# Kernel tuning notes

Measured on AMD Instinct MI355X. Metric: run time of the kernel, lower is better.

Reference implementation:

```python
import jax, jax.numpy as jnp
import numpy as np

D = 1024; H = 16; DH = 64; L = 4; N0 = 512; N1 = 512; NF = 16; B = 4; FF = 2730
FUSION = -1; GLOBAL = -2

# static token-type masks (zorro=True path)
_tt = np.concatenate([np.zeros(N0, np.int64), np.ones(N1, np.int64), np.full(NF, FUSION, np.int64)])
_allowed = (_tt[:, None] == _tt[None, :]) | (_tt[:, None] == FUSION)
ATTN_MASK = jnp.asarray(~_allowed)  # True = masked, shape [N, N]
_rt = np.array([0, 1, FUSION, GLOBAL], np.int64)
_pool_allowed = (_rt[:, None] == _tt[None, :]) | (_rt[:, None] == GLOBAL)
POOL_MASK = jnp.asarray(~_pool_allowed)  # [4, N]


def setup_inputs() -> dict:
    key = jax.random.key(0)
    ks = jax.random.split(key, 14)
    s = 0.02
    return {
        'm0': jax.random.normal(ks[0], (B, N0, D), jnp.float32),
        'm1': jax.random.normal(ks[1], (B, N1, D), jnp.float32),
        'fusion_tokens': jax.random.normal(ks[2], (NF, D), jnp.float32),
        'return_tokens': jax.random.normal(ks[3], (4, D), jnp.float32),
        'ln_gamma': jnp.ones((L, D), jnp.float32),
        'wq': jax.random.normal(ks[4], (L, D, H * DH), jnp.float32) * s,
        'wkv': jax.random.normal(ks[5], (L, D, 2 * H * DH), jnp.float32) * s,
        'wo': jax.random.normal(ks[6], (L, H * DH, D), jnp.float32) * s,
        'ff_w1': jax.random.normal(ks[7], (L, D, 2 * FF), jnp.float32) * s,
        'ff_w2': jax.random.normal(ks[8], (L, FF, D), jnp.float32) * s,
        'pool_wq': jax.random.normal(ks[9], (D, H * DH), jnp.float32) * s,
        'pool_wkv': jax.random.normal(ks[10], (D, 2 * H * DH), jnp.float32) * s,
        'pool_wo': jax.random.normal(ks[11], (H * DH, D), jnp.float32) * s,
        'final_gamma': jnp.ones((D,), jnp.float32),
    }


def _ln(x, g):
    mu = jnp.mean(x, axis=-1, keepdims=True)
    var = jnp.mean(jnp.square(x - mu), axis=-1, keepdims=True)
    return (x - mu) * jax.lax.rsqrt(var + 1e-5) * g


def _heads(t):  # [b, n, h*d] -> [b, h, n, d]
    b, n, _ = t.shape
    return t.reshape(b, n, H, DH).transpose(0, 2, 1, 3)


def _attn(x, ctx, wq, wkv, wo, mask):
    q = _heads(x @ wq) * (DH ** -0.5)
    k, v = map(_heads, jnp.split(ctx @ wkv, 2, axis=-1))
    sim = jnp.einsum('bhid,bhjd->bhij', q, k)
    sim = jnp.where(mask, -jnp.finfo(sim.dtype).max, sim)
    attn = jax.nn.softmax(sim, axis=-1)
    out = jnp.einsum('bhij,bhjd->bhid', attn, v)
    b, h, n, d = out.shape
    return out.transpose(0, 2, 1, 3).reshape(b, n, h * d) @ wo


def _ff(x, w1, w2):
    val, gate = jnp.split(x @ w1, 2, axis=-1)
    return (jax.nn.gelu(gate, approximate=False) * val) @ w2


def reference(m0, m1, fusion_tokens, return_tokens, ln_gamma, wq, wkv, wo, ff_w1, ff_w2, pool_wq, pool_wkv, pool_wo, final_gamma):
    b = m0.shape[0]
    fus = jnp.broadcast_to(fusion_tokens[None], (b, NF, D))
    tokens = jnp.concatenate([m0, m1, fus], axis=1)  # [B, N, D]
    for l in range(L):
        h = _ln(tokens, ln_gamma[l])
        tokens = _attn(h, h, wq[l], wkv[l], wo[l], ATTN_MASK) + tokens
        h = _ln(tokens, ln_gamma[l])
        tokens = _ff(h, ff_w1[l], ff_w2[l]) + tokens
    tokens = _ln(tokens, final_gamma)
    q = jnp.broadcast_to(return_tokens[None], (b, 4, D))
    pooled = _attn(q, tokens, pool_wq, pool_wkv, pool_wo, POOL_MASK) + return_tokens[None]
    return pooled
```

## Files before the change

kernel.cpp:

```cpp
#include <hip/hip_runtime.h>
#include <stdint.h>


#define DEV __device__ __forceinline__

typedef unsigned short u16;
typedef __attribute__((ext_vector_type(8))) __bf16 bf16x8;
typedef __attribute__((ext_vector_type(4))) float floatx4;

DEV u16 f2bf(float f) {
  union { float f; unsigned u; } v; v.f = f;
  return (u16)((v.u + 0x7fffu + ((v.u >> 16) & 1u)) >> 16);
}
DEV float bf2f(u16 s) {
  union { unsigned u; float f; } v; v.u = ((unsigned)s) << 16;
  return v.f;
}

#define MFMA(a, b, c) __builtin_amdgcn_mfma_f32_16x16x32_bf16(a, b, c, 0, 0, 0)

DEV void gld16(const u16* g, u16* l) {
  __builtin_amdgcn_global_load_lds((__attribute__((address_space(1))) void*)g,
                                   (__attribute__((address_space(3))) void*)l,
                                   16, 0, 0);
}

DEV int vperm32(int j) {
  return (((j >> 2) & 3) << 3) | (j & 3) | (((j >> 4) & 1) << 2);
}

#define MREAL 4160
#define MPAD  4224
#define NPAD  1056
#define FFP   2816
#define FF2P  5632

__global__ __launch_bounds__(256) void transpose_cvt(
    const float* __restrict__ in, u16* __restrict__ out,
    int Kin, int N, int Kstride) {
  __shared__ float tile[32][33];
  const int k0 = blockIdx.x * 32, n0 = blockIdx.y * 32;
  const int tx = threadIdx.x, ty = threadIdx.y;
#pragma unroll
  for (int i = 0; i < 4; i++) {
    int k = k0 + ty + i * 8;
    tile[ty + i * 8][tx] = (k < Kin) ? in[(int64_t)k * N + n0 + tx] : 0.f;
  }
  __syncthreads();
#pragma unroll
  for (int i = 0; i < 4; i++) {
    int n = n0 + ty + i * 8;
    int k = k0 + tx;
    if (k < Kstride) out[(int64_t)n * Kstride + k] = f2bf(tile[tx][ty + i * 8]);
  }
}

__global__ __launch_bounds__(256) void transpose_w1(
    const float* __restrict__ in, u16* __restrict__ out) {
  __shared__ float tile[32][33];
  const int k0 = blockIdx.x * 32;
  const int r0 = blockIdx.y * 32;
  const int tx = threadIdx.x, ty = threadIdx.y;
  const int vb = (r0 >> 5) << 4;
  const int vi = vb + (tx & 15);
  const int c = (tx < 16) ? vi : 2730 + vi;
  const bool valid = vi < 2730;
#pragma unroll
  for (int i = 0; i < 4; i++) {
    int k = k0 + ty + i * 8;
    tile[ty + i * 8][tx] = valid ? in[(int64_t)k * 5460 + c] : 0.f;
  }
  __syncthreads();
#pragma unroll
  for (int i = 0; i < 4; i++) {
    int rl = ty + i * 8;
    out[(int64_t)(r0 + rl) * 1024 + k0 + tx] = f2bf(tile[tx][rl]);
  }
}

__global__ __launch_bounds__(256) void build_tokens_k(
    const float* __restrict__ m0p, const float* __restrict__ m1p,
    const float* __restrict__ fus, float* __restrict__ tokens) {
  const int n = blockIdx.x, b = blockIdx.y, t = threadIdx.x;
  const float* src = (n < 512) ? m0p + ((int64_t)b * 512 + n) * 1024
                   : (n < 1024) ? m1p + ((int64_t)b * 512 + (n - 512)) * 1024
                                : fus + (int64_t)(n - 1024) * 1024;
  float4 v = ((const float4*)src)[t];
  ((float4*)(tokens + ((int64_t)b * 1040 + n) * 1024))[t] = v;
}

__global__ __launch_bounds__(256) void ln_k(const float* __restrict__ x,
                                            const float* __restrict__ gamma,
                                            u16* __restrict__ out) {
  const int r = blockIdx.x, t = threadIdx.x;
  const float4 v = ((const float4*)(x + (int64_t)r * 1024))[t];
  float s = v.x + v.y + v.z + v.w;
  float q = v.x * v.x + v.y * v.y + v.z * v.z + v.w * v.w;
#pragma unroll
  for (int off = 32; off >= 1; off >>= 1) {
    s += __shfl_xor(s, off);
    q += __shfl_xor(q, off);
  }
  __shared__ float red[8];
  const int w = t >> 6, l = t & 63;
  if (l == 0) { red[w] = s; red[4 + w] = q; }
  __syncthreads();
  s = red[0] + red[1] + red[2] + red[3];
  q = red[4] + red[5] + red[6] + red[7];
  const float mu = s * (1.f / 1024.f);
  const float var = q * (1.f / 1024.f) - mu * mu;
  const float rs = rsqrtf(var + 1e-5f);
  const float4 g = ((const float4*)gamma)[t];
  u16* op = out + (int64_t)r * 1024 + t * 4;
  op[0] = f2bf((v.x - mu) * rs * g.x);
  op[1] = f2bf((v.y - mu) * rs * g.y);
  op[2] = f2bf((v.z - mu) * rs * g.z);
  op[3] = f2bf((v.w - mu) * rs * g.w);
}

enum { EPI_QKV = 0, EPI_KV = 1, EPI_TOKADD = 2, EPI_GG = 3 };

template <int EPI>
__global__ __launch_bounds__(256) void gemm_bt(
    const u16* __restrict__ A, const u16* __restrict__ Bt,
    int Kstr, int Mreal,
    float* __restrict__ tokens, u16* __restrict__ oq, u16* __restrict__ ok,
    u16* __restrict__ ovT, u16* __restrict__ oh2) {
  __shared__ __align__(16) u16 lA0[128 * 32];
  __shared__ __align__(16) u16 lA1[128 * 32];
  __shared__ __align__(16) u16 lB0[128 * 32];
  __shared__ __align__(16) u16 lB1[128 * 32];
  const int t = threadIdx.x;
  const int w = t >> 6, l = t & 63;
  const int lane16 = l & 15, quad = l >> 4;
  const int m0 = blockIdx.y * 128, n0 = blockIdx.x * 128;
  const int wm = (w >> 1) * 64, wn = (w & 1) * 64;

  const int Klen = Kstr / gridDim.z;
  const int koff = blockIdx.z * Klen;

  const floatx4 fz = {0.f, 0.f, 0.f, 0.f};
  floatx4 acc[4][4];
#pragma unroll
  for (int i = 0; i < 4; i++)
#pragma unroll
    for (int j = 0; j < 4; j++) acc[i][j] = fz;

  const int rowL = t >> 2;
  const int colL = (t & 3) * 8;
  const u16* gA = A + (int64_t)(m0 + rowL) * Kstr + koff + colL;
  const u16* gB = Bt + (int64_t)(n0 + rowL) * Kstr + koff + colL;
  u16* lA0p = lA0 + t * 8;
  u16* lA1p = lA1 + t * 8;
  u16* lB0p = lB0 + t * 8;
  u16* lB1p = lB1 + t * 8;
  const int fo = (wm + lane16) * 32 + quad * 8;
  const int fon = (wn + lane16) * 32 + quad * 8;
  const int64_t rsk = (int64_t)64 * Kstr;

  for (int kt = 0; kt < Klen; kt += 64) {
    gld16(gA + kt, lA0p);
    gld16(gA + kt + rsk, lA0p + 64 * 32);
    gld16(gA + kt + 32, lA1p);
    gld16(gA + kt + 32 + rsk, lA1p + 64 * 32);
    gld16(gB + kt, lB0p);
    gld16(gB + kt + rsk, lB0p + 64 * 32);
    gld16(gB + kt + 32, lB1p);
    gld16(gB + kt + 32 + rsk, lB1p + 64 * 32);
    __syncthreads();
    bf16x8 af[4], bf[4];
#pragma unroll
    for (int i = 0; i < 4; i++) af[i] = *(const bf16x8*)(lA0 + fo + i * 16 * 32);
#pragma unroll
    for (int j = 0; j < 4; j++) bf[j] = *(const bf16x8*)(lB0 + fon + j * 16 * 32);
#pragma unroll
    for (int i = 0; i < 4; i++)
#pragma unroll
      for (int j = 0; j < 4; j++) acc[i][j] = MFMA(af[i], bf[j], acc[i][j]);
#pragma unroll
    for (int i = 0; i < 4; i++) af[i] = *(const bf16x8*)(lA1 + fo + i * 16 * 32);
#pragma unroll
    for (int j = 0; j < 4; j++) bf[j] = *(const bf16x8*)(lB1 + fon + j * 16 * 32);
#pragma unroll
    for (int i = 0; i < 4; i++)
#pragma unroll
      for (int j = 0; j < 4; j++) acc[i][j] = MFMA(af[i], bf[j], acc[i][j]);
    __syncthreads();
  }

  if constexpr (EPI == EPI_TOKADD) {
    const bool atomic = gridDim.z > 1;
#pragma unroll
    for (int i = 0; i < 4; i++) {
      const int mb = m0 + wm + i * 16 + quad * 4;
#pragma unroll
      for (int reg = 0; reg < 4; reg++) {
        const int m = mb + reg;
        if (m < Mreal) {
          float* tp = tokens + (int64_t)m * 1024;
#pragma unroll
          for (int j = 0; j < 4; j++) {
            const int n = n0 + wn + j * 16 + lane16;
            if (atomic) atomicAdd(tp + n, acc[i][j][reg]);
            else tp[n] += acc[i][j][reg];
          }
        }
      }
    }
  } else if constexpr (EPI == EPI_QKV) {
#pragma unroll
    for (int i = 0; i < 4; i++) {
      const int mb = m0 + wm + i * 16 + quad * 4;
#pragma unroll
      for (int reg = 0; reg < 4; reg++) {
        const int m = mb + reg;
        if (m < Mreal) {
          const int b = m / 1040, rb = m % 1040;
          const int rbp = (rb & ~31) | vperm32(rb & 31);
#pragma unroll
          for (int j = 0; j < 4; j++) {
            const int n = n0 + wn + j * 16 + lane16;
            const float v = acc[i][j][reg];
            if (n < 1024) {
              const int hd = n >> 6, d = n & 63;
              oq[(((int64_t)b * 16 + hd) * NPAD + rb) * 64 + d] = f2bf(v * 0.125f);
            } else if (n < 2048) {
              const int n2 = n - 1024;
              const int hd = n2 >> 6, d = n2 & 63;
              ok[(((int64_t)b * 16 + hd) * NPAD + rb) * 64 + d] = f2bf(v);
            } else {
              const int n2 = n - 2048;
              const int hd = n2 >> 6, d = n2 & 63;
              ovT[(((int64_t)b * 16 + hd) * 64 + d) * NPAD + rbp] = f2bf(v);
            }
          }
        }
      }
    }
  } else if constexpr (EPI == EPI_KV) {
#pragma unroll
    for (int i = 0; i < 4; i++) {
      const int mb = m0 + wm + i * 16 + quad * 4;
#pragma unroll
      for (int reg = 0; reg < 4; reg++) {
        const int m = mb + reg;
        if (m < Mreal) {
          const int b = m / 1040, rb = m % 1040;
          const int rbp = (rb & ~31) | vperm32(rb & 31);
#pragma unroll
          for (int j = 0; j < 4; j++) {
            const int n = n0 + wn + j * 16 + lane16;
            const float v = acc[i][j][reg];
            if (n < 1024) {
              const int hd = n >> 6, d = n & 63;
              ok[(((int64_t)b * 16 + hd) * NPAD + rb) * 64 + d] = f2bf(v);
            } else {
              const int n2 = n - 1024;
              const int hd = n2 >> 6, d = n2 & 63;
              ovT[(((int64_t)b * 16 + hd) * 64 + d) * NPAD + rbp] = f2bf(v);
            }
          }
        }
      }
    }
  } else {
#pragma unroll
    for (int i = 0; i < 4; i++) {
      const int mb = m0 + wm + i * 16 + quad * 4;
#pragma unroll
      for (int reg = 0; reg < 4; reg++) {
        const int m = mb + reg;
        u16* hp = oh2 + (int64_t)m * FFP;
#pragma unroll
        for (int j = 0; j < 4; j += 2) {
          const float val = acc[i][j][reg];
          const float g = acc[i][j + 1][reg];
          const float ge = 0.5f * g * (1.f + erff(g * 0.70710678118654752f));
          const int vi = (((n0 + wn + j * 16) >> 5) << 4) + lane16;
          hp[vi] = f2bf(val * ge);
        }
      }
    }
  }
}

__global__ __launch_bounds__(256) void attn_k(const u16* __restrict__ qb,
                                              const u16* __restrict__ kb,
                                              const u16* __restrict__ vTb,
                                              u16* __restrict__ ao) {
  const int t = threadIdx.x, w = t >> 6, l = t & 63;
  const int lane16 = l & 15, quad = l >> 4;
  const int kvb = quad * 4;
  const int bh = blockIdx.y, b = bh >> 4, h = bh & 15;
  const int row0 = blockIdx.x * 64 + w * 16;
  if (row0 >= 1040) return;
  const int type = (row0 < 512) ? 0 : (row0 < 1024 ? 1 : 2);
  const int cbeg = (type == 1) ? 512 : 0;
  const int cend = (type == 0) ? 512 : (type == 1 ? 1024 : 1040);
  const int niter = (cend - cbeg + 31) >> 5;

  const u16* qp = qb + ((int64_t)bh * NPAD + row0 + lane16) * 64 + quad * 8;
  const bf16x8 a0 = *(const bf16x8*)qp;
  const bf16x8 a1 = *(const bf16x8*)(qp + 32);
  const u16* vbase = vTb + ((int64_t)bh * 64 + lane16) * NPAD + quad * 8;

  const floatx4 fz = {0.f, 0.f, 0.f, 0.f};
  floatx4 O[4] = {fz, fz, fz, fz};
  float mrow = -1e30f, lrow = 0.f;

  for (int it = 0; it < niter; ++it) {
    const int c0 = cbeg + it * 32;
    const u16* kp = kb + ((int64_t)bh * NPAD + c0 + lane16) * 64 + quad * 8;
    const bf16x8 b00 = *(const bf16x8*)kp;
    const bf16x8 b01 = *(const bf16x8*)(kp + 32);
    const bf16x8 b10 = *(const bf16x8*)(kp + 16 * 64);
    const bf16x8 b11 = *(const bf16x8*)(kp + 16 * 64 + 32);
    floatx4 s0 = MFMA(b00, a0, fz); s0 = MFMA(b01, a1, s0);
    floatx4 s1 = MFMA(b10, a0, fz); s1 = MFMA(b11, a1, s1);
    if (c0 + 32 > cend) {
#pragma unroll
      for (int r = 0; r < 4; r++) {
        if (c0 + kvb + r >= cend) s0[r] = -1e30f;
        if (c0 + 16 + kvb + r >= cend) s1[r] = -1e30f;
      }
    }
    float tm = fmaxf(fmaxf(fmaxf(s0[0], s0[1]), fmaxf(s0[2], s0[3])),
                     fmaxf(fmaxf(s1[0], s1[1]), fmaxf(s1[2], s1[3])));
    tm = fmaxf(tm, __shfl_xor(tm, 16));
    tm = fmaxf(tm, __shfl_xor(tm, 32));
    if (!__all(tm <= mrow)) {
      const float mn = fmaxf(mrow, tm);
      const float a_ = __expf(mrow - mn);
      mrow = mn;
      lrow *= a_;
      const float al0 = __shfl(a_, kvb + 0, 16);
      const float al1 = __shfl(a_, kvb + 1, 16);
      const float al2 = __shfl(a_, kvb + 2, 16);
      const float al3 = __shfl(a_, kvb + 3, 16);
#pragma unroll
      for (int dt = 0; dt < 4; dt++) {
        O[dt][0] *= al0; O[dt][1] *= al1; O[dt][2] *= al2; O[dt][3] *= al3;
      }
    }
    float p0[4], p1[4];
#pragma unroll
    for (int r = 0; r < 4; r++) {
      p0[r] = __expf(s0[r] - mrow);
      p1[r] = __expf(s1[r] - mrow);
    }
    float ps = ((p0[0] + p0[1]) + (p0[2] + p0[3])) +
               ((p1[0] + p1[1]) + (p1[2] + p1[3]));
    ps += __shfl_xor(ps, 16);
    ps += __shfl_xor(ps, 32);
    lrow += ps;
    union { bf16x8 v; u16 s[8]; } pf;
#pragma unroll
    for (int r = 0; r < 4; r++) {
      pf.s[r] = f2bf(p0[r]);
      pf.s[4 + r] = f2bf(p1[r]);
    }
#pragma unroll
    for (int dt = 0; dt < 4; dt++) {
      const bf16x8 bv = *(const bf16x8*)(vbase + (int64_t)dt * 16 * NPAD + c0);
      O[dt] = MFMA(pf.v, bv, O[dt]);
    }
  }
  float lr[4];
#pragma unroll
  for (int r = 0; r < 4; r++) lr[r] = __shfl(lrow, kvb + r, 16);
#pragma unroll
  for (int dt = 0; dt < 4; dt++)
#pragma unroll
    for (int r = 0; r < 4; r++) {
      const int row = row0 + kvb + r;
      ao[((int64_t)b * 1040 + row) * 1024 + h * 64 + dt * 16 + lane16] =
          f2bf(O[dt][r] / lr[r]);
    }
}

__global__ __launch_bounds__(256) void poolq_k(const float* __restrict__ rtk,
                                               const float* __restrict__ pwq,
                                               u16* __restrict__ qP) {
  const int r = blockIdx.y;
  const int n = blockIdx.x * 256 + threadIdx.x;
  if (r >= 4) { qP[(int64_t)r * 1024 + n] = 0; return; }
  const float* x = rtk + (int64_t)r * 1024;
  float acc = 0.f;
#pragma unroll 8
  for (int k = 0; k < 1024; k++) acc += x[k] * pwq[(int64_t)k * 1024 + n];
  qP[(int64_t)r * 1024 + n] = f2bf(acc * 0.125f);
}

DEV bool pvalid(int r, int c) {
  if (r == 0) return c < 512;
  if (r == 1) return (c >= 512) && (c < 1024);
  if (r == 2) return (c >= 1024) && (c < 1040);
  return c < 1040;
}

__global__ __launch_bounds__(64) void pool_attn_k(const u16* __restrict__ qP,
                                                  const u16* __restrict__ kb,
                                                  const u16* __restrict__ vTb,
                                                  u16* __restrict__ po) {
  const int l = threadIdx.x;
  const int lane16 = l & 15, quad = l >> 4;
  const int kvb = quad * 4;
  const int bh = blockIdx.x, b = bh >> 4, h = bh & 15;
  const u16* qp = qP + (int64_t)lane16 * 1024 + h * 64 + quad * 8;
  const bf16x8 a0 = *(const bf16x8*)qp;
  const bf16x8 a1 = *(const bf16x8*)(qp + 32);
  const u16* vbase = vTb + ((int64_t)bh * 64 + lane16) * NPAD + quad * 8;
  const floatx4 fz = {0.f, 0.f, 0.f, 0.f};
  floatx4 O[4] = {fz, fz, fz, fz};
  float mrow = -1e30f, lrow = 0.f;
  for (int it = 0; it < 33; ++it) {
    const int c0 = it * 32;
    const u16* kp = kb + ((int64_t)bh * NPAD + c0 + lane16) * 64 + quad * 8;
    const bf16x8 b00 = *(const bf16x8*)kp;
    const bf16x8 b01 = *(const bf16x8*)(kp + 32);
    const bf16x8 b10 = *(const bf16x8*)(kp + 16 * 64);
    const bf16x8 b11 = *(const bf16x8*)(kp + 16 * 64 + 32);
    floatx4 s0 = MFMA(b00, a0, fz); s0 = MFMA(b01, a1, s0);
    floatx4 s1 = MFMA(b10, a0, fz); s1 = MFMA(b11, a1, s1);
#pragma unroll
    for (int r = 0; r < 4; r++) {
      if (!pvalid(lane16, c0 + kvb + r)) s0[r] = -1e30f;
      if (!pvalid(lane16, c0 + 16 + kvb + r)) s1[r] = -1e30f;
    }
    float tm = fmaxf(fmaxf(fmaxf(s0[0], s0[1]), fmaxf(s0[2], s0[3])),
                     fmaxf(fmaxf(s1[0], s1[1]), fmaxf(s1[2], s1[3])));
    tm = fmaxf(tm, __shfl_xor(tm, 16));
    tm = fmaxf(tm, __shfl_xor(tm, 32));
    if (!__all(tm <= mrow)) {
      const float mn = fmaxf(mrow, tm);
      const float a_ = __expf(mrow - mn);
      mrow = mn;
      lrow *= a_;
      const float al0 = __shfl(a_, kvb + 0, 16);
      const float al1 = __shfl(a_, kvb + 1, 16);
      const float al2 = __shfl(a_, kvb + 2, 16);
      const float al3 = __shfl(a_, kvb + 3, 16);
#pragma unroll
      for (int dt = 0; dt < 4; dt++) {
        O[dt][0] *= al0; O[dt][1] *= al1; O[dt][2] *= al2; O[dt][3] *= al3;
      }
    }
    float p0[4], p1[4];
#pragma unroll
    for (int r = 0; r < 4; r++) {
      p0[r] = __expf(s0[r] - mrow);
      p1[r] = __expf(s1[r] - mrow);
    }
    float ps = ((p0[0] + p0[1]) + (p0[2] + p0[3])) +
               ((p1[0] + p1[1]) + (p1[2] + p1[3]));
    ps += __shfl_xor(ps, 16);
    ps += __shfl_xor(ps, 32);
    lrow += ps;
    union { bf16x8 v; u16 s[8]; } pf;
#pragma unroll
    for (int r = 0; r < 4; r++) {
      pf.s[r] = f2bf(p0[r]);
      pf.s[4 + r] = f2bf(p1[r]);
    }
#pragma unroll
    for (int dt = 0; dt < 4; dt++) {
      const bf16x8 bv = *(const bf16x8*)(vbase + (int64_t)dt * 16 * NPAD + c0);
      O[dt] = MFMA(pf.v, bv, O[dt]);
    }
  }
  float lr[4];
#pragma unroll
  for (int r = 0; r < 4; r++) lr[r] = __shfl(lrow, r, 16);
  if (quad == 0) {
#pragma unroll
    for (int dt = 0; dt < 4; dt++)
#pragma unroll
      for (int r = 0; r < 4; r++)
        po[((int64_t)b * 4 + r) * 1024 + h * 64 + dt * 16 + lane16] =
            f2bf(O[dt][r] / lr[r]);
  }
}

__global__ __launch_bounds__(256) void fout_k(const u16* __restrict__ po,
                                              const float* __restrict__ pwo,
                                              const float* __restrict__ rtk,
                                              float* __restrict__ out) {
  const int row = blockIdx.y;
  const int n = blockIdx.x * 256 + threadIdx.x;
  const u16* x = po + (int64_t)row * 1024;
  float acc = 0.f;
#pragma unroll 8
  for (int k = 0; k < 1024; k++) acc += bf2f(x[k]) * pwo[(int64_t)k * 1024 + n];
  out[(int64_t)row * 1024 + n] = acc + rtk[(int64_t)(row & 3) * 1024 + n];
}

extern "C" void kernel_launch(void* const* d_in, const int* in_sizes, int n_in,
                              void* d_out, int out_size, void* d_ws, size_t ws_size,
                              hipStream_t stream) {
  (void)in_sizes; (void)n_in; (void)out_size; (void)ws_size;
  const float* m0p  = (const float*)d_in[0];
  const float* m1p  = (const float*)d_in[1];
  const float* fus  = (const float*)d_in[2];
  const float* rtk  = (const float*)d_in[3];
  const float* lng  = (const float*)d_in[4];
  const float* wq   = (const float*)d_in[5];
  const float* wkv  = (const float*)d_in[6];
  const float* wo   = (const float*)d_in[7];
  const float* w1   = (const float*)d_in[8];
  const float* w2   = (const float*)d_in[9];
  const float* pwq  = (const float*)d_in[10];
  const float* pwkv = (const float*)d_in[11];
  const float* pwo  = (const float*)d_in[12];
  const float* fg   = (const float*)d_in[13];
  float* out = (float*)d_out;

  char* p = (char*)d_ws;
  auto alloc = [&](size_t bytes) -> char* {
    char* r = p;
    p += (bytes + 255) & ~(size_t)255;
    return r;
  };
  u16* warena = (u16*)alloc((size_t)FF2P * 1024 * 2);
  float* tokens = (float*)alloc((size_t)MREAL * 1024 * 4);
  u16* hbuf  = (u16*)alloc((size_t)MPAD * 1024 * 2);
  u16* qb    = (u16*)alloc((size_t)64 * NPAD * 64 * 2);
  u16* kbuf  = (u16*)alloc((size_t)64 * NPAD * 64 * 2);
  u16* vTbuf = (u16*)alloc((size_t)64 * NPAD * 64 * 2);
  u16* h2buf = qb;
  u16* qP    = (u16*)alloc((size_t)16 * 1024 * 2);
  u16* poolO = (u16*)alloc((size_t)16 * 1024 * 2);

  const dim3 tb(32, 8, 1);
  build_tokens_k<<<dim3(1040, 4), 256, 0, stream>>>(m0p, m1p, fus, tokens);

  for (int lyr = 0; lyr < 4; ++lyr) {
    ln_k<<<MREAL, 256, 0, stream>>>(tokens, lng + lyr * 1024, hbuf);
    transpose_cvt<<<dim3(32, 32), tb, 0, stream>>>(
        wq + (int64_t)lyr * 1024 * 1024, warena, 1024, 1024, 1024);
    transpose_cvt<<<dim3(32, 64), tb, 0, stream>>>(
        wkv + (int64_t)lyr * 1024 * 2048, warena + (size_t)1024 * 1024, 1024, 2048, 1024);
    gemm_bt<EPI_QKV><<<dim3(24, 33), 256, 0, stream>>>(
        hbuf, warena, 1024, MREAL, nullptr, qb, kbuf, vTbuf, nullptr);
    attn_k<<<dim3(17, 64), 256, 0, stream>>>(qb, kbuf, vTbuf, hbuf);
    transpose_cvt<<<dim3(32, 32), tb, 0, stream>>>(
        wo + (int64_t)lyr * 1024 * 1024, warena, 1024, 1024, 1024);
    gemm_bt<EPI_TOKADD><<<dim3(8, 33, 2), 256, 0, stream>>>(
        hbuf, warena, 1024, MREAL, tokens, nullptr, nullptr, nullptr, nullptr);
    ln_k<<<MREAL, 256, 0, stream>>>(tokens, lng + lyr * 1024, hbuf);
    transpose_w1<<<dim3(32, FF2P / 32), tb, 0, stream>>>(
        w1 + (int64_t)lyr * 1024 * 5460, warena);
    gemm_bt<EPI_GG><<<dim3(FF2P / 128, 33), 256, 0, stream>>>(
        hbuf, warena, 1024, MREAL, nullptr, nullptr, nullptr, nullptr, h2buf);
    transpose_cvt<<<dim3(FFP / 32, 32), tb, 0, stream>>>(
        w2 + (int64_t)lyr * 2730 * 1024, warena, 2730, 1024, FFP);
    gemm_bt<EPI_TOKADD><<<dim3(8, 33, 2), 256, 0, stream>>>(
        h2buf, warena, FFP, MREAL, tokens, nullptr, nullptr, nullptr, nullptr);
  }

  ln_k<<<MREAL, 256, 0, stream>>>(tokens, fg, hbuf);
  transpose_cvt<<<dim3(32, 64), tb, 0, stream>>>(pwkv, warena, 1024, 2048, 1024);
  gemm_bt<EPI_KV><<<dim3(16, 33), 256, 0, stream>>>(
      hbuf, warena, 1024, MREAL, nullptr, nullptr, kbuf, vTbuf, nullptr);
  poolq_k<<<dim3(4, 16), 256, 0, stream>>>(rtk, pwq, qP);
  pool_attn_k<<<64, 64, 0, stream>>>(qP, kbuf, vTbuf, poolO);
  fout_k<<<dim3(4, 16), 256, 0, stream>>>(poolO, pwo, rtk, out);
}
```

Baseline: 1.859 ms.

## Double-buffer GEMM LDS tiles with XOR-swizzled layout to overlap loads

Replaces the single-stage LDS staging in the bf16 GEMM with two 128x64 buffers, prefetching the next K tile through global_load_lds while MFMAs run on the current one. The LDS layout changes to 64-element rows with an XOR swizzle on 16-byte chunks to cut bank conflicts on fragment reads. LDS use doubles to 64KB per block, which may lower occupancy. Only one barrier per iteration remains, so correctness depends on the asynchronous LDS loads completing before the barrier.

```diff
diff --git a/kernel.cpp b/kernel.cpp
--- a/kernel.cpp
+++ b/kernel.cpp
@@ -126,10 +126,8 @@
     int Kstr, int Mreal,
     float* __restrict__ tokens, u16* __restrict__ oq, u16* __restrict__ ok,
     u16* __restrict__ ovT, u16* __restrict__ oh2) {
-  __shared__ __align__(16) u16 lA0[128 * 32];
-  __shared__ __align__(16) u16 lA1[128 * 32];
-  __shared__ __align__(16) u16 lB0[128 * 32];
-  __shared__ __align__(16) u16 lB1[128 * 32];
+  __shared__ __align__(16) u16 lA[2][128 * 64];
+  __shared__ __align__(16) u16 lB[2][128 * 64];
   const int t = threadIdx.x;
   const int w = t >> 6, l = t & 63;
   const int lane16 = l & 15, quad = l >> 4;
@@ -146,46 +144,54 @@
 #pragma unroll
     for (int j = 0; j < 4; j++) acc[i][j] = fz;
 
-  const int rowL = t >> 2;
-  const int colL = (t & 3) * 8;
-  const u16* gA = A + (int64_t)(m0 + rowL) * Kstr + koff + colL;
-  const u16* gB = Bt + (int64_t)(n0 + rowL) * Kstr + koff + colL;
-  u16* lA0p = lA0 + t * 8;
-  u16* lA1p = lA1 + t * 8;
-  u16* lB0p = lB0 + t * 8;
-  u16* lB1p = lB1 + t * 8;
-  const int fo = (wm + lane16) * 32 + quad * 8;
-  const int fon = (wn + lane16) * 32 + quad * 8;
-  const int64_t rsk = (int64_t)64 * Kstr;
-
+  const int rowS = t >> 3;
+  const int scol = (((t & 7) ^ (rowS & 7)) << 3);
+  const u16* gAs = A + (int64_t)(m0 + rowS) * Kstr + koff + scol;
+  const u16* gBs = Bt + (int64_t)(n0 + rowS) * Kstr + koff + scol;
+  const int64_t csk = (int64_t)32 * Kstr;
+
+  const int rsw = lane16 & 7;
+  const int cp0 = ((quad ^ rsw) << 3);
+  const int cp1 = (((quad + 4) ^ rsw) << 3);
+
+  auto stage = [&](int buf, int kt) {
+    const u16* ga = gAs + kt;
+    const u16* gb = gBs + kt;
+    u16* la = &lA[buf][0] + t * 8;
+    u16* lb = &lB[buf][0] + t * 8;
+#pragma unroll
+    for (int c = 0; c < 4; c++) {
+      gld16(ga + c * csk, la + c * 2048);
+      gld16(gb + c * csk, lb + c * 2048);
+    }
+  };
+
+  stage(0, 0);
+  __syncthreads();
+  int cur = 0;
   for (int kt = 0; kt < Klen; kt += 64) {
-    gld16(gA + kt, lA0p);
-    gld16(gA + kt + rsk, lA0p + 64 * 32);
-    gld16(gA + kt + 32, lA1p);
-    gld16(gA + kt + 32 + rsk, lA1p + 64 * 32);
-    gld16(gB + kt, lB0p);
-    gld16(gB + kt + rsk, lB0p + 64 * 32);
-    gld16(gB + kt + 32, lB1p);
-    gld16(gB + kt + 32 + rsk, lB1p + 64 * 32);
-    __syncthreads();
+    if (kt + 64 < Klen) stage(cur ^ 1, kt + 64);
+    const u16* la = &lA[cur][0] + (wm + lane16) * 64;
+    const u16* lb = &lB[cur][0] + (wn + lane16) * 64;
     bf16x8 af[4], bf[4];
 #pragma unroll
-    for (int i = 0; i < 4; i++) af[i] = *(const bf16x8*)(lA0 + fo + i * 16 * 32);
-#pragma unroll
-    for (int j = 0; j < 4; j++) bf[j] = *(const bf16x8*)(lB0 + fon + j * 16 * 32);
+    for (int i = 0; i < 4; i++) af[i] = *(const bf16x8*)(la + i * 16 * 64 + cp0);
+#pragma unroll
+    for (int j = 0; j < 4; j++) bf[j] = *(const bf16x8*)(lb + j * 16 * 64 + cp0);
 #pragma unroll
     for (int i = 0; i < 4; i++)
 #pragma unroll
       for (int j = 0; j < 4; j++) acc[i][j] = MFMA(af[i], bf[j], acc[i][j]);
 #pragma unroll
-    for (int i = 0; i < 4; i++) af[i] = *(const bf16x8*)(lA1 + fo + i * 16 * 32);
-#pragma unroll
-    for (int j = 0; j < 4; j++) bf[j] = *(const bf16x8*)(lB1 + fon + j * 16 * 32);
+    for (int i = 0; i < 4; i++) af[i] = *(const bf16x8*)(la + i * 16 * 64 + cp1);
+#pragma unroll
+    for (int j = 0; j < 4; j++) bf[j] = *(const bf16x8*)(lb + j * 16 * 64 + cp1);
 #pragma unroll
     for (int i = 0; i < 4; i++)
 #pragma unroll
       for (int j = 0; j < 4; j++) acc[i][j] = MFMA(af[i], bf[j], acc[i][j]);
     __syncthreads();
+    cur ^= 1;
   }
 
   if constexpr (EPI == EPI_TOKADD) {
```

New measurement: 1.877 ms. No clear change (+1.0%).
